# Kernel optimization log

Hardware: AMD Instinct MI355X
Metric: run time of the kernel (lower is better)

Reference implementation:

```python
import jax, jax.numpy as jnp
import numpy as np

B, S, HIST, D, NH, L = 8, 1024, 128, 1024, 16, 6
SD, TD, AD = 10, 3, 5
DH = D // NH
FF = 4 * D
EPS = 1e-5
SCALE = 1.0 / np.sqrt(DH)


def posenc(T):
    # sinusoidal PE, matches PositionalEncoding (positions start at 0)
    pos = jnp.arange(T, dtype=jnp.float32)[:, None]
    div = jnp.exp(jnp.arange(0, D, 2, dtype=jnp.float32) * (-np.log(10000.0) / D))
    pe = jnp.zeros((T, D), jnp.float32)
    pe = pe.at[:, 0::2].set(jnp.sin(pos * div))
    pe = pe.at[:, 1::2].set(jnp.cos(pos * div))
    return pe


def layernorm(x, g, b):
    m = jnp.mean(x, -1, keepdims=True)
    v = jnp.var(x, -1, keepdims=True)
    return (x - m) * jax.lax.rsqrt(v + EPS) * g + b


def mlp2(u, w1, b1, w2, b2):
    # Linear -> SiLU -> Linear (ConditionEmbedding branch)
    return jax.nn.silu(u @ w1 + b1) @ w2 + b2


def mha(q_in, kv_in, wq, bq, wk, bk, wv, bv, wo, bo, mask):
    Bq, Tq, _ = q_in.shape
    Tk = kv_in.shape[1]
    q = (q_in @ wq + bq).reshape(Bq, Tq, NH, DH)
    k = (kv_in @ wk + bk).reshape(Bq, Tk, NH, DH)
    v = (kv_in @ wv + bv).reshape(Bq, Tk, NH, DH)
    s = jnp.einsum('bthd,bshd->bhts', q, k) * SCALE + mask
    a = jax.nn.softmax(s, axis=-1)
    o = jnp.einsum('bhts,bshd->bthd', a, v).reshape(Bq, Tq, D)
    return o @ wo + bo


def setup_inputs():
    key = jax.random.key(0)
    ki = iter(jax.random.split(key, 64))
    w = lambda *sh: jax.random.normal(next(ki), sh, jnp.float32) * 0.02
    z = lambda *sh: jnp.zeros(sh, jnp.float32)
    inp = {
        'x': jax.random.normal(next(ki), (B, S, SD), jnp.float32),
        't': jax.random.randint(next(ki), (B,), 0, 30, dtype=jnp.int32),
        'target': jax.random.normal(next(ki), (B, TD), jnp.float32),
        'action': jax.random.normal(next(ki), (B, AD), jnp.float32),
        'history': jax.random.normal(next(ki), (B, HIST, SD), jnp.float32),
        'in_w': w(SD, D), 'in_b': z(D),
        't_w1': w(1, D), 't_b1': z(D), 't_w2': w(D, D), 't_b2': z(D),
        'tg_w1': w(TD, D), 'tg_b1': z(D), 'tg_w2': w(D, D), 'tg_b2': z(D),
        'ac_w1': w(AD, D), 'ac_b1': z(D), 'ac_w2': w(D, D), 'ac_b2': z(D),
        'sa_wq': w(L, D, D), 'sa_bq': z(L, D), 'sa_wk': w(L, D, D), 'sa_bk': z(L, D),
        'sa_wv': w(L, D, D), 'sa_bv': z(L, D), 'sa_wo': w(L, D, D), 'sa_bo': z(L, D),
        'ca_wq': w(L, D, D), 'ca_bq': z(L, D), 'ca_wk': w(L, D, D), 'ca_bk': z(L, D),
        'ca_wv': w(L, D, D), 'ca_bv': z(L, D), 'ca_wo': w(L, D, D), 'ca_bo': z(L, D),
        'ln1_g': jnp.ones((L, D), jnp.float32), 'ln1_b': z(L, D),
        'ln2_g': jnp.ones((L, D), jnp.float32), 'ln2_b': z(L, D),
        'ln3_g': jnp.ones((L, D), jnp.float32), 'ln3_b': z(L, D),
        'ff_w1': w(L, D, FF), 'ff_b1': z(L, FF), 'ff_w2': w(L, FF, D), 'ff_b2': z(L, D),
        'out_w': w(D, SD), 'out_b': z(SD),
    }
    return inp


def reference(x, t, target, action, history, in_w, in_b,
              t_w1, t_b1, t_w2, t_b2, tg_w1, tg_b1, tg_w2, tg_b2,
              ac_w1, ac_b1, ac_w2, ac_b2,
              sa_wq, sa_bq, sa_wk, sa_bk, sa_wv, sa_bv, sa_wo, sa_bo,
              ca_wq, ca_bq, ca_wk, ca_bk, ca_wv, ca_bv, ca_wo, ca_bo,
              ln1_g, ln1_b, ln2_g, ln2_b, ln3_g, ln3_b,
              ff_w1, ff_b1, ff_w2, ff_b2, out_w, out_b):
    # embed current traj and history (PE applied to each separately, as in torch code)
    x_emb = x @ in_w + in_b + posenc(S)[None]
    h_emb = history @ in_w + in_b + posenc(HIST)[None]
    # condition embedding: t + target + action branches
    cond = (mlp2(t[:, None].astype(jnp.float32), t_w1, t_b1, t_w2, t_b2)
            + mlp2(target, tg_w1, tg_b1, tg_w2, tg_b2)
            + mlp2(action, ac_w1, ac_b1, ac_w2, ac_b2))
    z = jnp.concatenate([h_emb, x_emb], axis=1) + cond[:, None, :]  # [B, T, D]
    T = HIST + S
    mask = jnp.where(jnp.tril(jnp.ones((T, T), bool)), 0.0, -jnp.inf)[None, None]
    mem = z  # TransformerDecoder memory is the (fixed) input sequence
    for i in range(L):
        # post-LN TransformerDecoderLayer: self-attn, cross-attn, relu FFN
        z = layernorm(z + mha(z, z, sa_wq[i], sa_bq[i], sa_wk[i], sa_bk[i],
                              sa_wv[i], sa_bv[i], sa_wo[i], sa_bo[i], mask), ln1_g[i], ln1_b[i])
        z = layernorm(z + mha(z, mem, ca_wq[i], ca_bq[i], ca_wk[i], ca_bk[i],
                              ca_wv[i], ca_bv[i], ca_wo[i], ca_bo[i], mask), ln2_g[i], ln2_b[i])
        ff = jax.nn.relu(z @ ff_w1[i] + ff_b1[i]) @ ff_w2[i] + ff_b2[i]
        z = layernorm(z + ff, ln3_g[i], ln3_b[i])
    return z[:, -S:, :] @ out_w + out_b
```

## Files before the change

### kernel.cpp

```cpp
#include <hip/hip_runtime.h>
#include <hip/hip_bf16.h>
#include <stdint.h>

#define B_    8
#define S_    1024
#define HIST_ 128
#define T_    1152
#define D_    1024
#define NH_   16
#define DH_   64
#define FF_   4096
#define L_    6
#define NROWS_ (B_*T_)

typedef __attribute__((ext_vector_type(8))) __bf16 bf16x8;
typedef __attribute__((ext_vector_type(4))) __bf16 bf16x4;
typedef __attribute__((ext_vector_type(4))) float  f32x4;

static __device__ __forceinline__ f32x4 mfma16(bf16x8 a, bf16x8 b, f32x4 c) {
  return __builtin_amdgcn_mfma_f32_16x16x32_bf16(a, b, c, 0, 0, 0);
}
static __device__ __forceinline__ void gload16(const __bf16* g, __bf16* l) {
  __builtin_amdgcn_global_load_lds((const __attribute__((address_space(1))) void*)g,
                                   (__attribute__((address_space(3))) void*)l, 16, 0, 0);
}
static __device__ __forceinline__ void gload16b(const char* g, char* l) {
  __builtin_amdgcn_global_load_lds((const __attribute__((address_space(1))) void*)g,
                                   (__attribute__((address_space(3))) void*)l, 16, 0, 0);
}
static __device__ __forceinline__ int xcd_swz(int orig, int nwg) {
  const int q = nwg >> 3, r = nwg & 7;
  const int x = orig & 7, i = orig >> 3;
  return (x < r ? x*(q+1) : r*(q+1) + (x-r)*q) + i;
}

template<int OUTMODE, int RELU>
__global__ __launch_bounds__(512, 2) void gemm256_k(const __bf16* __restrict__ A,
                                                    const __bf16* __restrict__ A2, int asplit,
                                                    const __bf16* __restrict__ Bt,
                                                    const float* __restrict__ b1,
                                                    const float* __restrict__ b2,
                                                    const float* __restrict__ b3, int s1, int s2,
                                                    void* __restrict__ CoutRM,
                                                    __bf16* __restrict__ CoutT,
                                                    int M, int N, int K, int ldc, int tsplit) {
  __shared__ __align__(16) __bf16 Lds[2][2][2][8192];
  const int tid = threadIdx.x;
  const int wid = tid >> 6, ln = tid & 63;
  const int wm = wid >> 2, wn = wid & 3;
  const int l15 = ln & 15, g = ln >> 4;
  const int nbx = N >> 8;
  const int wg = xcd_swz(blockIdx.x, gridDim.x);
  const int m0 = (wg / nbx) << 8, n0 = (wg % nbx) << 8;
  const size_t rstep = (size_t)K * 2;
  const __bf16* Aeff = (n0 < asplit) ? A : A2;

  const int srow = tid >> 2, schunk = tid & 3;
  const int sx = (schunk ^ ((srow >> 1) & 3)) << 4;
  const char* gAr = (const char*)Aeff + (size_t)(m0 + srow)*rstep + sx;
  const char* gBr = (const char*)Bt   + (size_t)(n0 + srow)*rstep + sx;
  const size_t hstep = (size_t)128 * rstep;

  const int xr = (g ^ ((l15 >> 1) & 3)) << 4;
  const int arow = l15 * 64 + xr;
  const int aoffm = (wm*128) * 64;
  const int boff  = (wn*64) * 64;

  const f32x4 zero = {0.f,0.f,0.f,0.f};
  f32x4 acc[8][4];
#pragma unroll
  for (int i=0;i<8;i++)
#pragma unroll
    for (int j=0;j<4;j++) acc[i][j] = zero;

  auto stage4 = [&](int buf, int ks, int tile) {
    const size_t off = (size_t)tile*128 + (size_t)ks*64;
    char* la = (char*)&Lds[buf][ks][0][0];
    char* lb = (char*)&Lds[buf][ks][1][0];
    gload16b(gAr + off,         la + tid*16);
    gload16b(gAr + off + hstep, la + 8192 + tid*16);
    gload16b(gBr + off,         lb + tid*16);
    gload16b(gBr + off + hstep, lb + 8192 + tid*16);
  };

  auto ktile = [&](int buf, bool st, int stile, bool gate0) {
    if (gate0) { asm volatile("s_waitcnt vmcnt(0)" ::: "memory"); }
    else       { asm volatile("s_waitcnt vmcnt(8)" ::: "memory"); }
    __builtin_amdgcn_s_barrier();
    const char* As0 = (const char*)&Lds[buf][0][0][0];
    const char* Bs0 = (const char*)&Lds[buf][0][1][0];
    const char* As1 = (const char*)&Lds[buf][1][0][0];
    const char* Bs1 = (const char*)&Lds[buf][1][1][0];
    bf16x8 a0[4], a1[4], b0[4], a2[4], b1v[4], a3[4];
#pragma unroll
    for (int mi=0;mi<4;mi++) a0[mi] = *(const bf16x8*)(As0 + aoffm + mi*1024 + arow);
#pragma unroll
    for (int ni=0;ni<4;ni++) b0[ni] = *(const bf16x8*)(Bs0 + boff + ni*1024 + arow);
#pragma unroll
    for (int mi=0;mi<4;mi++) a1[mi] = *(const bf16x8*)(As0 + aoffm + 4096 + mi*1024 + arow);
    __builtin_amdgcn_s_setprio(1);
#pragma unroll
    for (int mi=0;mi<4;mi++)
#pragma unroll
      for (int ni=0;ni<4;ni++) acc[mi][ni] = mfma16(a0[mi], b0[ni], acc[mi][ni]);
    __builtin_amdgcn_s_setprio(0);
#pragma unroll
    for (int mi=0;mi<4;mi++) a2[mi]  = *(const bf16x8*)(As1 + aoffm + mi*1024 + arow);
#pragma unroll
    for (int ni=0;ni<4;ni++) b1v[ni] = *(const bf16x8*)(Bs1 + boff + ni*1024 + arow);
    asm volatile("s_waitcnt lgkmcnt(0)" ::: "memory");
    __builtin_amdgcn_s_barrier();
    if (st) stage4(buf, 0, stile);
    __builtin_amdgcn_s_setprio(1);
#pragma unroll
    for (int mi=0;mi<4;mi++)
#pragma unroll
      for (int ni=0;ni<4;ni++) acc[4+mi][ni] = mfma16(a1[mi], b0[ni], acc[4+mi][ni]);
    __builtin_amdgcn_s_setprio(0);
#pragma unroll
    for (int mi=0;mi<4;mi++) a3[mi] = *(const bf16x8*)(As1 + aoffm + 4096 + mi*1024 + arow);
    __builtin_amdgcn_s_setprio(1);
#pragma unroll
    for (int mi=0;mi<4;mi++)
#pragma unroll
      for (int ni=0;ni<4;ni++) acc[mi][ni] = mfma16(a2[mi], b1v[ni], acc[mi][ni]);
    __builtin_amdgcn_s_setprio(0);
    asm volatile("s_waitcnt lgkmcnt(0)" ::: "memory");
    __builtin_amdgcn_s_barrier();
    if (st) stage4(buf, 1, stile);
    __builtin_amdgcn_s_setprio(1);
#pragma unroll
    for (int mi=0;mi<4;mi++)
#pragma unroll
      for (int ni=0;ni<4;ni++) acc[4+mi][ni] = mfma16(a3[mi], b1v[ni], acc[4+mi][ni]);
    __builtin_amdgcn_s_setprio(0);
  };

  stage4(0, 0, 0); stage4(0, 1, 0);
  stage4(1, 0, 1); stage4(1, 1, 1);

  const int NT = K >> 6, NI = NT >> 1;
  for (int i = 0; i < NI; ++i) {
    const bool st = (i + 1 < NI);
    ktile(0, st, 2*i + 2, false);
    ktile(1, st, 2*i + 3, i == NI - 1);
  }

  const int colb = n0 + wn*64 + l15;
#pragma unroll
  for (int mi=0;mi<8;mi++) {
    const int row = m0 + wm*128 + mi*16 + g*4;
#pragma unroll
    for (int ni=0;ni<4;ni++) {
      const int col = colb + ni*16;
      const float bv = (col < s1) ? b1[col] : ((col < s2) ? b2[col-s1] : b3[col-s2]);
      if (OUTMODE == 3 && col >= tsplit) {
        bf16x4 ct;
#pragma unroll
        for (int j=0;j<4;j++) {
          float v = acc[mi][ni][j] + bv;
          if (RELU) v = fmaxf(v, 0.f);
          ct[j] = (__bf16)v;
        }
        *(bf16x4*)(CoutT + (size_t)(col - tsplit)*M + row) = ct;
      } else {
#pragma unroll
        for (int j=0;j<4;j++) {
          float v = acc[mi][ni][j] + bv;
          if (RELU) v = fmaxf(v, 0.f);
          if (OUTMODE == 0) ((float*)CoutRM)[(size_t)(row+j)*ldc + col] = v;
          else              ((__bf16*)CoutRM)[(size_t)(row+j)*ldc + col] = (__bf16)v;
        }
      }
    }
  }
}

__global__ __launch_bounds__(256) void attn_k(const __bf16* __restrict__ QK,
                                              const __bf16* __restrict__ Vt,
                                              __bf16* __restrict__ O) {
  __shared__ __align__(16) __bf16 Ks[2][4096];
  __shared__ __align__(16) __bf16 Vs[2][4096];
  __shared__ __align__(16) __bf16 Pl[4][32*72];
  const int tid = threadIdx.x;
  const int wv = tid >> 6, ln = tid & 63;
  const int l15 = ln & 15, g = ln >> 4;
  const int wg = xcd_swz(blockIdx.x, 1152);
  const int qb = 8 - (wg % 9);
  const int hd = (wg / 9) & 15;
  const int b  = wg / 144;
  const int q0 = qb*128 + wv*32;

  bf16x8 qf[2][2];
#pragma unroll
  for (int f=0; f<2; ++f)
#pragma unroll
    for (int h=0; h<2; ++h)
      qf[f][h] = *(const bf16x8*)(QK + (size_t)(b*T_ + q0 + f*16 + l15)*2048 + hd*64 + h*32 + g*8);

  const int sr = tid >> 3;
  const int si = tid & 7;
  const int cb0 = (si*16) ^ ((sr & 7) << 4);
  const char* kg = (const char*)(QK + (size_t)b*T_*2048 + 1024 + hd*64);
  const char* vg = (const char*)(Vt + (size_t)hd*64*NROWS_ + (size_t)b*T_);

  const f32x4 zero = {0.f,0.f,0.f,0.f};
  f32x4 o[2][4];
#pragma unroll
  for (int f=0; f<2; ++f)
#pragma unroll
    for (int d=0; d<4; ++d) o[f][d] = zero;
  float mrun[2] = {-3.0e38f, -3.0e38f};
  float lrun[2] = {0.f, 0.f};
  const int nt = 2*qb + 2;

  {
    const int c = 0, kt = 0;
#pragma unroll
    for (int hr=0; hr<2; ++hr) {
      const int r = sr + hr*32;
      gload16((const __bf16*)(kg + (size_t)(kt + r)*4096 + cb0), &Ks[c][0] + hr*2048 + wv*512);
      gload16((const __bf16*)(vg + (size_t)r*(NROWS_*2) + (size_t)kt*2 + cb0), &Vs[c][0] + hr*2048 + wv*512);
    }
  }

  for (int t = 0; t < nt; ++t) {
    __syncthreads();
    if (t+1 < nt) {
      const int c = (t+1)&1, kt2 = (t+1)*64;
#pragma unroll
      for (int hr=0; hr<2; ++hr) {
        const int r = sr + hr*32;
        gload16((const __bf16*)(kg + (size_t)(kt2 + r)*4096 + cb0), &Ks[c][0] + hr*2048 + wv*512);
        gload16((const __bf16*)(vg + (size_t)r*(NROWS_*2) + (size_t)kt2*2 + cb0), &Vs[c][0] + hr*2048 + wv*512);
      }
    }
    const int kt = t*64;
    if (kt > q0 + 31) continue;
    const char* ks = (const char*)&Ks[t&1][0];
    const char* vs = (const char*)&Vs[t&1][0];

#pragma unroll
    for (int f=0; f<2; ++f) {
      const int qrow = q0 + f*16 + l15;
      f32x4 st[4];
      __builtin_amdgcn_s_setprio(1);
#pragma unroll
      for (int kf=0; kf<4; ++kf) {
        const int row = kf*16 + l15;
        const int swz = (row & 7) << 4;
        const bf16x8 k0 = *(const bf16x8*)(ks + row*128 + ((g*16) ^ swz));
        const bf16x8 k1 = *(const bf16x8*)(ks + row*128 + ((64 + g*16) ^ swz));
        st[kf] = mfma16(k1, qf[f][1], mfma16(k0, qf[f][0], zero));
      }
      __builtin_amdgcn_s_setprio(0);
      float p[16];
#pragma unroll
      for (int kf=0; kf<4; ++kf)
#pragma unroll
        for (int r=0; r<4; ++r) {
          const int kgl = kt + kf*16 + g*4 + r;
          p[kf*4+r] = (kgl <= qrow) ? st[kf][r]*0.125f : -3.0e38f;
        }
      float mloc = p[0];
#pragma unroll
      for (int i=1;i<16;i++) mloc = fmaxf(mloc, p[i]);
      mloc = fmaxf(mloc, __shfl_xor(mloc, 16));
      mloc = fmaxf(mloc, __shfl_xor(mloc, 32));
      if (__all(mloc - mrun[f] <= 8.f)) {
        float ls = 0.f;
#pragma unroll
        for (int i=0;i<16;i++) { p[i] = __expf(p[i] - mrun[f]); ls += p[i]; }
        ls += __shfl_xor(ls, 16); ls += __shfl_xor(ls, 32);
        lrun[f] += ls;
      } else {
        const float mnew = fmaxf(mrun[f], mloc);
        const float corr = __expf(mrun[f] - mnew);
        float ls = 0.f;
#pragma unroll
        for (int i=0;i<16;i++) { p[i] = __expf(p[i] - mnew); ls += p[i]; }
        ls += __shfl_xor(ls, 16); ls += __shfl_xor(ls, 32);
        lrun[f] = lrun[f]*corr + ls;
        mrun[f] = mnew;
        float cr[4];
#pragma unroll
        for (int r=0;r<4;r++) cr[r] = __shfl(corr, g*4 + r);
#pragma unroll
        for (int db=0; db<4; ++db)
#pragma unroll
          for (int r=0;r<4;r++) o[f][db][r] *= cr[r];
      }
#pragma unroll
      for (int kf=0; kf<4; ++kf) {
        bf16x4 pw;
#pragma unroll
        for (int r=0;r<4;r++) pw[r] = (__bf16)p[kf*4+r];
        *(bf16x4*)(&Pl[wv][(f*16 + l15)*72 + kf*16 + g*4]) = pw;
      }
    }
    __builtin_amdgcn_s_setprio(1);
#pragma unroll
    for (int f=0; f<2; ++f)
#pragma unroll
      for (int ks2=0; ks2<2; ++ks2) {
        const bf16x8 pa = *(const bf16x8*)(&Pl[wv][(f*16 + l15)*72 + ks2*32 + g*8]);
#pragma unroll
        for (int db=0; db<4; ++db) {
          const int d = db*16 + l15;
          const bf16x8 vf = *(const bf16x8*)(vs + d*128 + ((ks2*64 + g*16) ^ ((d & 7) << 4)));
          o[f][db] = mfma16(pa, vf, o[f][db]);
        }
      }
    __builtin_amdgcn_s_setprio(0);
  }

#pragma unroll
  for (int f=0; f<2; ++f) {
    const float inv = 1.f / lrun[f];
    float ir[4];
#pragma unroll
    for (int r=0;r<4;r++) ir[r] = __shfl(inv, g*4 + r);
#pragma unroll
    for (int db=0; db<4; ++db)
#pragma unroll
      for (int r=0;r<4;r++)
        O[(size_t)(b*T_ + q0 + f*16 + g*4 + r)*D_ + hd*64 + db*16 + l15] = (__bf16)(o[f][db][r]*ir[r]);
  }
}

__global__ __launch_bounds__(256) void wprep_k(const float* __restrict__ q, const float* __restrict__ k,
                                               const float* __restrict__ v, const float* __restrict__ o,
                                               const float* __restrict__ cq, const float* __restrict__ ck,
                                               const float* __restrict__ cv, const float* __restrict__ co,
                                               const float* __restrict__ f1, const float* __restrict__ f2,
                                               __bf16* __restrict__ wb) {
  __shared__ float tile[32][33];
  const int id = blockIdx.x;
  const float* src; __bf16* dst; int R, C, bx, by;
  if (id < 8192) {
    const int m = id >> 10, t = id & 1023; bx = t & 31; by = t >> 5;
    const float* srcs[8] = {q,k,v,o,cq,ck,cv,co};
    src = srcs[m]; dst = wb + (size_t)m*1048576; R = 1024; C = 1024;
  } else if (id < 12288) {
    const int t = id - 8192; bx = t & 127; by = t >> 7;
    src = f1; dst = wb + (size_t)8*1048576; R = 1024; C = 4096;
  } else {
    const int t = id - 12288; bx = t & 31; by = t >> 5;
    src = f2; dst = wb + (size_t)12*1048576; R = 4096; C = 1024;
  }
  const int tx = threadIdx.x & 31, ty = threadIdx.x >> 5;
  const int r0 = by*32, c0 = bx*32;
#pragma unroll
  for (int i=0;i<4;i++) tile[ty+i*8][tx] = src[(size_t)(r0+ty+i*8)*C + c0+tx];
  __syncthreads();
#pragma unroll
  for (int i=0;i<4;i++) dst[(size_t)(c0+ty+i*8)*R + r0+tx] = (__bf16)tile[tx][ty+i*8];
}

__global__ __launch_bounds__(256) void ln_k(const float* __restrict__ zin, const float* __restrict__ yin,
                                            const float* __restrict__ gam, const float* __restrict__ bet,
                                            float* __restrict__ zout, __bf16* __restrict__ zbout) {
  const int row = blockIdx.x, tid = threadIdx.x;
  const f32x4 zv = ((const f32x4*)(zin + (size_t)row*D_))[tid];
  const f32x4 yv = ((const f32x4*)(yin + (size_t)row*D_))[tid];
  f32x4 v = zv + yv;
  float s1 = v[0]+v[1]+v[2]+v[3];
  float s2 = v[0]*v[0]+v[1]*v[1]+v[2]*v[2]+v[3]*v[3];
#pragma unroll
  for (int off=32; off; off>>=1) { s1 += __shfl_xor(s1,off); s2 += __shfl_xor(s2,off); }
  __shared__ float red[8];
  const int wv = tid>>6, ln = tid&63;
  if (ln==0) { red[wv] = s1; red[4+wv] = s2; }
  __syncthreads();
  s1 = red[0]+red[1]+red[2]+red[3];
  s2 = red[4]+red[5]+red[6]+red[7];
  const float mean = s1 * (1.f/1024.f);
  const float var = s2 * (1.f/1024.f) - mean*mean;
  const float rs = rsqrtf(var + 1e-5f);
  const f32x4 gv = ((const f32x4*)gam)[tid];
  const f32x4 bv = ((const f32x4*)bet)[tid];
  f32x4 r; bf16x4 rb;
#pragma unroll
  for (int j=0;j<4;j++) { float t = (v[j]-mean)*rs*gv[j] + bv[j]; r[j] = t; rb[j] = (__bf16)t; }
  ((f32x4*)(zout + (size_t)row*D_))[tid] = r;
  ((bf16x4*)(zbout + (size_t)row*D_))[tid] = rb;
}

__global__ __launch_bounds__(256) void cond1_k(const int* __restrict__ t, const float* __restrict__ target,
                                               const float* __restrict__ action,
                                               const float* __restrict__ t_w1, const float* __restrict__ t_b1,
                                               const float* __restrict__ tg_w1, const float* __restrict__ tg_b1,
                                               const float* __restrict__ ac_w1, const float* __restrict__ ac_b1,
                                               float* __restrict__ h3) {
  const int i = blockIdx.x*256 + threadIdx.x;
  const int b = i >> 10, d = i & 1023;
  float u = (float)t[b] * t_w1[d] + t_b1[d];
  h3[i] = u / (1.f + __expf(-u));
  u = tg_b1[d];
#pragma unroll
  for (int j=0;j<3;j++) u += target[b*3+j]*tg_w1[j*1024+d];
  h3[8192 + i] = u / (1.f + __expf(-u));
  u = ac_b1[d];
#pragma unroll
  for (int j=0;j<5;j++) u += action[b*5+j]*ac_w1[j*1024+d];
  h3[16384 + i] = u / (1.f + __expf(-u));
}

__global__ __launch_bounds__(256) void cond2_k(const float* __restrict__ h3,
                                               const float* __restrict__ t_w2, const float* __restrict__ tg_w2,
                                               const float* __restrict__ ac_w2, float* __restrict__ cpart) {
  const int i = blockIdx.x*256 + threadIdx.x;
  const int ks = blockIdx.y;
  const int b = i >> 10, d = i & 1023;
  const float* ht = h3 + b*1024;
  const float* hg = h3 + 8192 + b*1024;
  const float* ha = h3 + 16384 + b*1024;
  float a = 0.f;
  for (int k = ks*128; k < ks*128+128; ++k)
    a += ht[k]*t_w2[(size_t)k*1024+d] + hg[k]*tg_w2[(size_t)k*1024+d] + ha[k]*ac_w2[(size_t)k*1024+d];
  cpart[ks*8192 + i] = a;
}

__global__ __launch_bounds__(256) void embed_k(const float* __restrict__ x, const float* __restrict__ hist,
                                               const float* __restrict__ in_w, const float* __restrict__ in_b,
                                               const float* __restrict__ cpart,
                                               const float* __restrict__ t_b2, const float* __restrict__ tg_b2,
                                               const float* __restrict__ ac_b2,
                                               float* __restrict__ z, __bf16* __restrict__ zb,
                                               __bf16* __restrict__ memb) {
  const int row = blockIdx.x, tid = threadIdx.x;
  const int b = row / T_, tt = row - b*T_;
  const float* feat = (tt < HIST_) ? (hist + ((size_t)b*HIST_ + tt)*10) : (x + ((size_t)b*S_ + (tt-HIST_))*10);
  float f[10];
#pragma unroll
  for (int s=0;s<10;s++) f[s] = feat[s];
  const float te = (float)((tt < HIST_) ? tt : tt - HIST_);
  f32x4 a = ((const f32x4*)in_b)[tid];
#pragma unroll
  for (int u=0;u<2;u++) {
    const int d = tid*4 + 2*u;
    const float freq = __expf((float)d * (-9.210340371976184f/1024.f));
    float sn, cs;
    __sincosf(te*freq, &sn, &cs);
    a[2*u] += sn; a[2*u+1] += cs;
  }
  a += ((const f32x4*)t_b2)[tid];
  a += ((const f32x4*)tg_b2)[tid];
  a += ((const f32x4*)ac_b2)[tid];
  const int cb = b*256 + tid;
#pragma unroll
  for (int ks=0;ks<8;ks++) a += ((const f32x4*)cpart)[ks*2048 + cb];
#pragma unroll
  for (int s=0;s<10;s++) {
    const f32x4 wv = ((const f32x4*)(in_w + s*1024))[tid];
    a += wv * f[s];
  }
  ((f32x4*)(z + (size_t)row*D_))[tid] = a;
  bf16x4 ab;
#pragma unroll
  for (int j=0;j<4;j++) ab[j] = (__bf16)a[j];
  ((bf16x4*)(zb + (size_t)row*D_))[tid] = ab;
  ((bf16x4*)(memb + (size_t)row*D_))[tid] = ab;
}

__global__ __launch_bounds__(256) void outp_k(const float* __restrict__ z, const float* __restrict__ w,
                                              const float* __restrict__ bo, float* __restrict__ out) {
  const int wv = threadIdx.x>>6, ln = threadIdx.x&63;
  const int row = blockIdx.x*4 + wv;
  const int b = row >> 10, s = row & 1023;
  const float* zr = z + ((size_t)b*T_ + HIST_ + s)*D_;
  float acc[10];
#pragma unroll
  for (int o=0;o<10;o++) acc[o]=0.f;
  for (int k=ln; k<1024; k+=64) {
    const float zv = zr[k];
    const float* wr = w + k*10;
#pragma unroll
    for (int o=0;o<10;o++) acc[o] += zv*wr[o];
  }
#pragma unroll
  for (int o=0;o<10;o++) {
#pragma unroll
    for (int off=32; off; off>>=1) acc[o] += __shfl_xor(acc[o], off);
  }
  if (ln==0) {
#pragma unroll
    for (int o=0;o<10;o++) out[(size_t)row*10+o] = acc[o] + bo[o];
  }
}

extern "C" void kernel_launch(void* const* d_in, const int* in_sizes, int n_in,
                              void* d_out, int out_size, void* d_ws, size_t ws_size,
                              hipStream_t stream) {
  const float* x      = (const float*)d_in[0];
  const int*   t      = (const int*)  d_in[1];
  const float* target = (const float*)d_in[2];
  const float* action = (const float*)d_in[3];
  const float* hist   = (const float*)d_in[4];
  const float* in_w   = (const float*)d_in[5];
  const float* in_b   = (const float*)d_in[6];
  const float* t_w1   = (const float*)d_in[7];
  const float* t_b1   = (const float*)d_in[8];
  const float* t_w2   = (const float*)d_in[9];
  const float* t_b2   = (const float*)d_in[10];
  const float* tg_w1  = (const float*)d_in[11];
  const float* tg_b1  = (const float*)d_in[12];
  const float* tg_w2  = (const float*)d_in[13];
  const float* tg_b2  = (const float*)d_in[14];
  const float* ac_w1  = (const float*)d_in[15];
  const float* ac_b1  = (const float*)d_in[16];
  const float* ac_w2  = (const float*)d_in[17];
  const float* ac_b2  = (const float*)d_in[18];
  const float* sa_wq  = (const float*)d_in[19];
  const float* sa_bq  = (const float*)d_in[20];
  const float* sa_wk  = (const float*)d_in[21];
  const float* sa_bk  = (const float*)d_in[22];
  const float* sa_wv  = (const float*)d_in[23];
  const float* sa_bv  = (const float*)d_in[24];
  const float* sa_wo  = (const float*)d_in[25];
  const float* sa_bo  = (const float*)d_in[26];
  const float* ca_wq  = (const float*)d_in[27];
  const float* ca_bq  = (const float*)d_in[28];
  const float* ca_wk  = (const float*)d_in[29];
  const float* ca_bk  = (const float*)d_in[30];
  const float* ca_wv  = (const float*)d_in[31];
  const float* ca_bv  = (const float*)d_in[32];
  const float* ca_wo  = (const float*)d_in[33];
  const float* ca_bo  = (const float*)d_in[34];
  const float* ln1_g  = (const float*)d_in[35];
  const float* ln1_b  = (const float*)d_in[36];
  const float* ln2_g  = (const float*)d_in[37];
  const float* ln2_b  = (const float*)d_in[38];
  const float* ln3_g  = (const float*)d_in[39];
  const float* ln3_b  = (const float*)d_in[40];
  const float* ff_w1  = (const float*)d_in[41];
  const float* ff_b1  = (const float*)d_in[42];
  const float* ff_w2  = (const float*)d_in[43];
  const float* ff_b2  = (const float*)d_in[44];
  const float* out_w  = (const float*)d_in[45];
  const float* out_b  = (const float*)d_in[46];

  if (ws_size < (size_t)224*1024*1024) return;

  char* p = (char*)d_ws;
  auto take = [&](size_t bytes) { char* r = p; p += (bytes + 255) & ~(size_t)255; return r; };
  __bf16* wbuf = (__bf16*)take((size_t)16*1024*1024*2);
  float*  z    = (float*) take((size_t)NROWS_*D_*4);
  __bf16* zb   = (__bf16*)take((size_t)NROWS_*D_*2);
  __bf16* memb = (__bf16*)take((size_t)NROWS_*D_*2);
  __bf16* qk   = (__bf16*)take((size_t)NROWS_*2048*2);
  __bf16* vt   = (__bf16*)take((size_t)1024*NROWS_*2);
  __bf16* ob   = (__bf16*)take((size_t)NROWS_*D_*2);
  float*  y    = (float*) take((size_t)NROWS_*D_*4);
  float*  h3   = (float*) take((size_t)3*8192*4);
  float*  cpart= (float*) take((size_t)8*8192*4);
  __bf16* ffh  = qk;

  const dim3 blk(256);
  const dim3 blk5(512);
  const int BIG = 1<<30;
  cond1_k<<<32, blk, 0, stream>>>(t, target, action, t_w1, t_b1, tg_w1, tg_b1, ac_w1, ac_b1, h3);
  cond2_k<<<dim3(32,8), blk, 0, stream>>>(h3, t_w2, tg_w2, ac_w2, cpart);
  embed_k<<<NROWS_, blk, 0, stream>>>(x, hist, in_w, in_b, cpart, t_b2, tg_b2, ac_b2, z, zb, memb);

  const int M = NROWS_;
  for (int li=0; li<L_; ++li) {
    const size_t w0 = (size_t)li*D_*D_, b0 = (size_t)li*D_;
    const size_t f1 = (size_t)li*D_*FF_, fb1 = (size_t)li*FF_;
    wprep_k<<<16384, blk, 0, stream>>>(sa_wq+w0, sa_wk+w0, sa_wv+w0, sa_wo+w0,
                                       ca_wq+w0, ca_wk+w0, ca_wv+w0, ca_wo+w0,
                                       ff_w1+f1, ff_w2+f1, wbuf);
    gemm256_k<3,0><<<36*12, blk5, 0, stream>>>(zb, zb, BIG, wbuf+0*1048576,
                                               sa_bq+b0, sa_bk+b0, sa_bv+b0, 1024, 2048,
                                               qk, vt, M, 3072, 1024, 2048, 2048);
    attn_k<<<1152, blk, 0, stream>>>(qk, vt, ob);
    gemm256_k<0,0><<<36*4, blk5, 0, stream>>>(ob, ob, BIG, wbuf+3*1048576,
                                              sa_bo+b0, sa_bo+b0, sa_bo+b0, BIG, BIG,
                                              y, vt, M, 1024, 1024, 1024, BIG);
    ln_k<<<NROWS_, blk, 0, stream>>>(z, y, ln1_g+b0, ln1_b+b0, z, zb);
    gemm256_k<3,0><<<36*12, blk5, 0, stream>>>(zb, memb, 1024, wbuf+4*1048576,
                                               ca_bq+b0, ca_bk+b0, ca_bv+b0, 1024, 2048,
                                               qk, vt, M, 3072, 1024, 2048, 2048);
    attn_k<<<1152, blk, 0, stream>>>(qk, vt, ob);
    gemm256_k<0,0><<<36*4, blk5, 0, stream>>>(ob, ob, BIG, wbuf+7*1048576,
                                              ca_bo+b0, ca_bo+b0, ca_bo+b0, BIG, BIG,
                                              y, vt, M, 1024, 1024, 1024, BIG);
    ln_k<<<NROWS_, blk, 0, stream>>>(z, y, ln2_g+b0, ln2_b+b0, z, zb);
    gemm256_k<1,1><<<36*16, blk5, 0, stream>>>(zb, zb, BIG, wbuf+(size_t)8*1048576,
                                               ff_b1+fb1, ff_b1+fb1, ff_b1+fb1, BIG, BIG,
                                               ffh, vt, M, 4096, 1024, 4096, BIG);
    gemm256_k<0,0><<<36*4, blk5, 0, stream>>>(ffh, ffh, BIG, wbuf+(size_t)12*1048576,
                                              ff_b2+b0, ff_b2+b0, ff_b2+b0, BIG, BIG,
                                              y, vt, M, 1024, 4096, 1024, BIG);
    ln_k<<<NROWS_, blk, 0, stream>>>(z, y, ln3_g+b0, ln3_b+b0, z, zb);
  }
  outp_k<<<2048, blk, 0, stream>>>(z, out_w, out_b, (float*)d_out);
}
```

Baseline: 4.354 ms.

## Add 192x256-tile GEMM for output/FFN projections and store residual branch in bf16

```diff
diff --git a/kernel.cpp b/kernel.cpp
--- a/kernel.cpp
+++ b/kernel.cpp
@@ -32,6 +32,112 @@
   const int q = nwg >> 3, r = nwg & 7;
   const int x = orig & 7, i = orig >> 3;
   return (x < r ? x*(q+1) : r*(q+1) + (x-r)*q) + i;
+}
+
+template<int BF16OUT, int RELU>
+__global__ __launch_bounds__(512, 2) void gemm192_k(const __bf16* __restrict__ A,
+                                                    const __bf16* __restrict__ Bt,
+                                                    const float* __restrict__ bias,
+                                                    void* __restrict__ Cout,
+                                                    int M, int N, int K, int ldc) {
+  __shared__ __align__(16) char Lds[2][57344];
+  const int tid = threadIdx.x;
+  const int wid = tid >> 6, ln = tid & 63;
+  const int wm = wid >> 2, wn = wid & 3;
+  const int l15 = ln & 15, g = ln >> 4;
+  const int nbx = N >> 8;
+  const int wg = xcd_swz(blockIdx.x, gridDim.x);
+  const int m0 = (wg / nbx) * 192, n0 = (wg % nbx) << 8;
+  const size_t rstep = (size_t)K * 2;
+
+  const char* srcp[7];
+  int dsto[7];
+#pragma unroll
+  for (int p = 0; p < 7; ++p) {
+    const int off = p*8192 + tid*16;
+    int mat, ks, row;
+    if (off < 12288)      { mat = 0; ks = 0; row = off >> 6; }
+    else if (off < 24576) { mat = 0; ks = 1; row = (off - 12288) >> 6; }
+    else if (off < 40960) { mat = 1; ks = 0; row = (off - 24576) >> 6; }
+    else                  { mat = 1; ks = 1; row = (off - 40960) >> 6; }
+    const int ch = (off >> 4) & 3;
+    const int kb = ks*64 + ((ch ^ ((row >> 1) & 3)) << 4);
+    srcp[p] = (mat ? (const char*)Bt + (size_t)(n0 + row)*rstep
+                   : (const char*)A  + (size_t)(m0 + row)*rstep) + kb;
+    dsto[p] = off;
+  }
+  auto stage = [&](int buf, int t) {
+    char* lb = &Lds[buf][0];
+    const size_t tb = (size_t)t << 7;
+#pragma unroll
+    for (int p = 0; p < 7; ++p) gload16b(srcp[p] + tb, lb + dsto[p]);
+  };
+
+  const int xr = (g ^ ((l15 >> 1) & 3)) << 4;
+  const int arow = l15*64 + xr;
+  const int aoffm = (wm*96) * 64;
+  const int boff  = 24576 + (wn*64) * 64;
+
+  const f32x4 zero = {0.f,0.f,0.f,0.f};
+  f32x4 acc[6][4];
+#pragma unroll
+  for (int i=0;i<6;i++)
+#pragma unroll
+    for (int j=0;j<4;j++) acc[i][j] = zero;
+
+  stage(0, 0); stage(1, 1);
+
+  const int NT = K >> 6;
+  for (int t = 0; t < NT; ++t) {
+    const int buf = t & 1;
+    if (t == NT-1) { asm volatile("s_waitcnt vmcnt(0)" ::: "memory"); }
+    else           { asm volatile("s_waitcnt vmcnt(7)" ::: "memory"); }
+    __builtin_amdgcn_s_barrier();
+    const char* bufp = &Lds[buf][0];
+    bf16x8 a0[6], a1[6], b0[4], b1[4];
+#pragma unroll
+    for (int mi=0;mi<6;mi++) a0[mi] = *(const bf16x8*)(bufp + aoffm + mi*1024 + arow);
+#pragma unroll
+    for (int ni=0;ni<4;ni++) b0[ni] = *(const bf16x8*)(bufp + boff + ni*1024 + arow);
+#pragma unroll
+    for (int mi=0;mi<6;mi++) a1[mi] = *(const bf16x8*)(bufp + 12288 + aoffm + mi*1024 + arow);
+    __builtin_amdgcn_s_setprio(1);
+#pragma unroll
+    for (int mi=0;mi<6;mi++)
+#pragma unroll
+      for (int ni=0;ni<4;ni++) acc[mi][ni] = mfma16(a0[mi], b0[ni], acc[mi][ni]);
+    __builtin_amdgcn_s_setprio(0);
+#pragma unroll
+    for (int ni=0;ni<4;ni++) b1[ni] = *(const bf16x8*)(bufp + boff + 16384 + ni*1024 + arow);
+    asm volatile("s_waitcnt lgkmcnt(0)" ::: "memory");
+    __builtin_amdgcn_sched_barrier(0);
+    __builtin_amdgcn_s_barrier();
+    if (t + 2 <= NT - 1) stage(buf, t + 2);
+    __builtin_amdgcn_s_setprio(1);
+#pragma unroll
+    for (int mi=0;mi<6;mi++)
+#pragma unroll
+      for (int ni=0;ni<4;ni++) acc[mi][ni] = mfma16(a1[mi], b1[ni], acc[mi][ni]);
+    __builtin_amdgcn_s_setprio(0);
+  }
+
+  const int colb = n0 + wn*64 + l15;
+#pragma unroll
+  for (int mi=0;mi<6;mi++) {
+    const int row = m0 + wm*96 + mi*16 + g*4;
+#pragma unroll
+    for (int ni=0;ni<4;ni++) {
+      const int col = colb + ni*16;
+      const float bv = bias[col];
+#pragma unroll
+      for (int j=0;j<4;j++) {
+        float v = acc[mi][ni][j] + bv;
+        if (RELU) v = fmaxf(v, 0.f);
+        if (BF16OUT) ((__bf16*)Cout)[(size_t)(row+j)*ldc + col] = (__bf16)v;
+        else         ((float*)Cout)[(size_t)(row+j)*ldc + col] = v;
+      }
+    }
+  }
 }
 
 template<int OUTMODE, int RELU>
@@ -357,13 +463,15 @@
   for (int i=0;i<4;i++) dst[(size_t)(c0+ty+i*8)*R + r0+tx] = (__bf16)tile[tx][ty+i*8];
 }
 
-__global__ __launch_bounds__(256) void ln_k(const float* __restrict__ zin, const float* __restrict__ yin,
+__global__ __launch_bounds__(256) void ln_k(const float* __restrict__ zin, const __bf16* __restrict__ yin,
                                             const float* __restrict__ gam, const float* __restrict__ bet,
                                             float* __restrict__ zout, __bf16* __restrict__ zbout) {
   const int row = blockIdx.x, tid = threadIdx.x;
   const f32x4 zv = ((const f32x4*)(zin + (size_t)row*D_))[tid];
-  const f32x4 yv = ((const f32x4*)(yin + (size_t)row*D_))[tid];
-  f32x4 v = zv + yv;
+  const bf16x4 yv4 = ((const bf16x4*)(yin + (size_t)row*D_))[tid];
+  f32x4 v;
+#pragma unroll
+  for (int j=0;j<4;j++) v[j] = zv[j] + (float)yv4[j];
   float s1 = v[0]+v[1]+v[2]+v[3];
   float s2 = v[0]*v[0]+v[1]*v[1]+v[2]*v[2]+v[3]*v[3];
 #pragma unroll
@@ -551,7 +659,7 @@
   __bf16* qk   = (__bf16*)take((size_t)NROWS_*2048*2);
   __bf16* vt   = (__bf16*)take((size_t)1024*NROWS_*2);
   __bf16* ob   = (__bf16*)take((size_t)NROWS_*D_*2);
-  float*  y    = (float*) take((size_t)NROWS_*D_*4);
+  __bf16* y    = (__bf16*)take((size_t)NROWS_*D_*2);
   float*  h3   = (float*) take((size_t)3*8192*4);
   float*  cpart= (float*) take((size_t)8*8192*4);
   __bf16* ffh  = qk;
@@ -574,24 +682,16 @@
                                                sa_bq+b0, sa_bk+b0, sa_bv+b0, 1024, 2048,
                                                qk, vt, M, 3072, 1024, 2048, 2048);
     attn_k<<<1152, blk, 0, stream>>>(qk, vt, ob);
-    gemm256_k<0,0><<<36*4, blk5, 0, stream>>>(ob, ob, BIG, wbuf+3*1048576,
-                                              sa_bo+b0, sa_bo+b0, sa_bo+b0, BIG, BIG,
-                                              y, vt, M, 1024, 1024, 1024, BIG);
+    gemm192_k<1,0><<<48*4, blk5, 0, stream>>>(ob, wbuf+3*1048576, sa_bo+b0, y, M, 1024, 1024, 1024);
     ln_k<<<NROWS_, blk, 0, stream>>>(z, y, ln1_g+b0, ln1_b+b0, z, zb);
     gemm256_k<3,0><<<36*12, blk5, 0, stream>>>(zb, memb, 1024, wbuf+4*1048576,
                                                ca_bq+b0, ca_bk+b0, ca_bv+b0, 1024, 2048,
                                                qk, vt, M, 3072, 1024, 2048, 2048);
     attn_k<<<1152, blk, 0, stream>>>(qk, vt, ob);
-    gemm256_k<0,0><<<36*4, blk5, 0, stream>>>(ob, ob, BIG, wbuf+7*1048576,
-                                              ca_bo+b0, ca_bo+b0, ca_bo+b0, BIG, BIG,
-                                              y, vt, M, 1024, 1024, 1024, BIG);
+    gemm192_k<1,0><<<48*4, blk5, 0, stream>>>(ob, wbuf+7*1048576, ca_bo+b0, y, M, 1024, 1024, 1024);
     ln_k<<<NROWS_, blk, 0, stream>>>(z, y, ln2_g+b0, ln2_b+b0, z, zb);
-    gemm256_k<1,1><<<36*16, blk5, 0, stream>>>(zb, zb, BIG, wbuf+(size_t)8*1048576,
-                                               ff_b1+fb1, ff_b1+fb1, ff_b1+fb1, BIG, BIG,
-                                               ffh, vt, M, 4096, 1024, 4096, BIG);
-    gemm256_k<0,0><<<36*4, blk5, 0, stream>>>(ffh, ffh, BIG, wbuf+(size_t)12*1048576,
-                                              ff_b2+b0, ff_b2+b0, ff_b2+b0, BIG, BIG,
-                                              y, vt, M, 1024, 4096, 1024, BIG);
+    gemm192_k<1,1><<<48*16, blk5, 0, stream>>>(zb, wbuf+(size_t)8*1048576, ff_b1+fb1, ffh, M, 4096, 1024, 4096);
+    gemm192_k<1,0><<<48*4, blk5, 0, stream>>>(ffh, wbuf+(size_t)12*1048576, ff_b2+b0, y, M, 1024, 4096, 1024);
     ln_k<<<NROWS_, blk, 0, stream>>>(z, y, ln3_g+b0, ln3_b+b0, z, zb);
   }
   outp_k<<<2048, blk, 0, stream>>>(z, out_w, out_b, (float*)d_out);
```

Result: faster. 3.947 ms (-9.4%).

## Switch GEMM to 192x256 tiles and store residual GEMM output in bf16

Applied to the files above, without the earlier changes.

```diff
diff --git a/kernel.cpp b/kernel.cpp
--- a/kernel.cpp
+++ b/kernel.cpp
@@ -35,7 +35,7 @@
 }
 
 template<int OUTMODE, int RELU>
-__global__ __launch_bounds__(512, 2) void gemm256_k(const __bf16* __restrict__ A,
+__global__ __launch_bounds__(512, 2) void gemm192_k(const __bf16* __restrict__ A,
                                                     const __bf16* __restrict__ A2, int asplit,
                                                     const __bf16* __restrict__ Bt,
                                                     const float* __restrict__ b1,
@@ -44,112 +44,92 @@
                                                     void* __restrict__ CoutRM,
                                                     __bf16* __restrict__ CoutT,
                                                     int M, int N, int K, int ldc, int tsplit) {
-  __shared__ __align__(16) __bf16 Lds[2][2][2][8192];
+  __shared__ __align__(16) char Lds[2][57344];
   const int tid = threadIdx.x;
   const int wid = tid >> 6, ln = tid & 63;
   const int wm = wid >> 2, wn = wid & 3;
   const int l15 = ln & 15, g = ln >> 4;
   const int nbx = N >> 8;
   const int wg = xcd_swz(blockIdx.x, gridDim.x);
-  const int m0 = (wg / nbx) << 8, n0 = (wg % nbx) << 8;
+  const int m0 = (wg / nbx) * 192, n0 = (wg % nbx) << 8;
   const size_t rstep = (size_t)K * 2;
   const __bf16* Aeff = (n0 < asplit) ? A : A2;
 
-  const int srow = tid >> 2, schunk = tid & 3;
-  const int sx = (schunk ^ ((srow >> 1) & 3)) << 4;
-  const char* gAr = (const char*)Aeff + (size_t)(m0 + srow)*rstep + sx;
-  const char* gBr = (const char*)Bt   + (size_t)(n0 + srow)*rstep + sx;
-  const size_t hstep = (size_t)128 * rstep;
+  const char* srcp[7];
+  int dsto[7];
+#pragma unroll
+  for (int p = 0; p < 7; ++p) {
+    const int off = p*8192 + tid*16;
+    int mat, ks, row;
+    if (off < 12288)      { mat = 0; ks = 0; row = off >> 6; }
+    else if (off < 24576) { mat = 0; ks = 1; row = (off - 12288) >> 6; }
+    else if (off < 40960) { mat = 1; ks = 0; row = (off - 24576) >> 6; }
+    else                  { mat = 1; ks = 1; row = (off - 40960) >> 6; }
+    const int ch = (off >> 4) & 3;
+    const int kb = ks*64 + ((ch ^ ((row >> 1) & 3)) << 4);
+    srcp[p] = (mat ? (const char*)Bt   + (size_t)(n0 + row)*rstep
+                   : (const char*)Aeff + (size_t)(m0 + row)*rstep) + kb;
+    dsto[p] = off;
+  }
+  auto stage = [&](int buf, int t) {
+    char* lb = &Lds[buf][0];
+    const size_t tb = (size_t)t << 7;
+#pragma unroll
+    for (int p = 0; p < 7; ++p) gload16b(srcp[p] + tb, lb + dsto[p]);
+  };
 
   const int xr = (g ^ ((l15 >> 1) & 3)) << 4;
-  const int arow = l15 * 64 + xr;
-  const int aoffm = (wm*128) * 64;
-  const int boff  = (wn*64) * 64;
+  const int arow = l15*64 + xr;
+  const int aoffm = (wm*96) * 64;
+  const int boff  = 24576 + (wn*64) * 64;
 
   const f32x4 zero = {0.f,0.f,0.f,0.f};
-  f32x4 acc[8][4];
-#pragma unroll
-  for (int i=0;i<8;i++)
+  f32x4 acc[6][4];
+#pragma unroll
+  for (int i=0;i<6;i++)
 #pragma unroll
     for (int j=0;j<4;j++) acc[i][j] = zero;
 
-  auto stage4 = [&](int buf, int ks, int tile) {
-    const size_t off = (size_t)tile*128 + (size_t)ks*64;
-    char* la = (char*)&Lds[buf][ks][0][0];
-    char* lb = (char*)&Lds[buf][ks][1][0];
-    gload16b(gAr + off,         la + tid*16);
-    gload16b(gAr + off + hstep, la + 8192 + tid*16);
-    gload16b(gBr + off,         lb + tid*16);
-    gload16b(gBr + off + hstep, lb + 8192 + tid*16);
-  };
-
-  auto ktile = [&](int buf, bool st, int stile, bool gate0) {
-    if (gate0) { asm volatile("s_waitcnt vmcnt(0)" ::: "memory"); }
-    else       { asm volatile("s_waitcnt vmcnt(8)" ::: "memory"); }
+  stage(0, 0); stage(1, 1);
+
+  const int NT = K >> 6;
+  for (int t = 0; t < NT; ++t) {
+    const int buf = t & 1;
+    if (t == NT-1) { asm volatile("s_waitcnt vmcnt(0)" ::: "memory"); }
+    else           { asm volatile("s_waitcnt vmcnt(7)" ::: "memory"); }
     __builtin_amdgcn_s_barrier();
-    const char* As0 = (const char*)&Lds[buf][0][0][0];
-    const char* Bs0 = (const char*)&Lds[buf][0][1][0];
-    const char* As1 = (const char*)&Lds[buf][1][0][0];
-    const char* Bs1 = (const char*)&Lds[buf][1][1][0];
-    bf16x8 a0[4], a1[4], b0[4], a2[4], b1v[4], a3[4];
-#pragma unroll
-    for (int mi=0;mi<4;mi++) a0[mi] = *(const bf16x8*)(As0 + aoffm + mi*1024 + arow);
-#pragma unroll
-    for (int ni=0;ni<4;ni++) b0[ni] = *(const bf16x8*)(Bs0 + boff + ni*1024 + arow);
-#pragma unroll
-    for (int mi=0;mi<4;mi++) a1[mi] = *(const bf16x8*)(As0 + aoffm + 4096 + mi*1024 + arow);
+    const char* bufp = &Lds[buf][0];
+    bf16x8 a0[6], a1[6], b0[4], b1[4];
+#pragma unroll
+    for (int mi=0;mi<6;mi++) a0[mi] = *(const bf16x8*)(bufp + aoffm + mi*1024 + arow);
+#pragma unroll
+    for (int ni=0;ni<4;ni++) b0[ni] = *(const bf16x8*)(bufp + boff + ni*1024 + arow);
+#pragma unroll
+    for (int mi=0;mi<6;mi++) a1[mi] = *(const bf16x8*)(bufp + 12288 + aoffm + mi*1024 + arow);
     __builtin_amdgcn_s_setprio(1);
 #pragma unroll
-    for (int mi=0;mi<4;mi++)
+    for (int mi=0;mi<6;mi++)
 #pragma unroll
       for (int ni=0;ni<4;ni++) acc[mi][ni] = mfma16(a0[mi], b0[ni], acc[mi][ni]);
     __builtin_amdgcn_s_setprio(0);
 #pragma unroll
-    for (int mi=0;mi<4;mi++) a2[mi]  = *(const bf16x8*)(As1 + aoffm + mi*1024 + arow);
-#pragma unroll
-    for (int ni=0;ni<4;ni++) b1v[ni] = *(const bf16x8*)(Bs1 + boff + ni*1024 + arow);
+    for (int ni=0;ni<4;ni++) b1[ni] = *(const bf16x8*)(bufp + boff + 16384 + ni*1024 + arow);
     asm volatile("s_waitcnt lgkmcnt(0)" ::: "memory");
+    __builtin_amdgcn_sched_barrier(0);
     __builtin_amdgcn_s_barrier();
-    if (st) stage4(buf, 0, stile);
+    if (t + 2 <= NT - 1) stage(buf, t + 2);
     __builtin_amdgcn_s_setprio(1);
 #pragma unroll
-    for (int mi=0;mi<4;mi++)
-#pragma unroll
-      for (int ni=0;ni<4;ni++) acc[4+mi][ni] = mfma16(a1[mi], b0[ni], acc[4+mi][ni]);
+    for (int mi=0;mi<6;mi++)
+#pragma unroll
+      for (int ni=0;ni<4;ni++) acc[mi][ni] = mfma16(a1[mi], b1[ni], acc[mi][ni]);
     __builtin_amdgcn_s_setprio(0);
-#pragma unroll
-    for (int mi=0;mi<4;mi++) a3[mi] = *(const bf16x8*)(As1 + aoffm + 4096 + mi*1024 + arow);
-    __builtin_amdgcn_s_setprio(1);
-#pragma unroll
-    for (int mi=0;mi<4;mi++)
-#pragma unroll
-      for (int ni=0;ni<4;ni++) acc[mi][ni] = mfma16(a2[mi], b1v[ni], acc[mi][ni]);
-    __builtin_amdgcn_s_setprio(0);
-    asm volatile("s_waitcnt lgkmcnt(0)" ::: "memory");
-    __builtin_amdgcn_s_barrier();
-    if (st) stage4(buf, 1, stile);
-    __builtin_amdgcn_s_setprio(1);
-#pragma unroll
-    for (int mi=0;mi<4;mi++)
-#pragma unroll
-      for (int ni=0;ni<4;ni++) acc[4+mi][ni] = mfma16(a3[mi], b1v[ni], acc[4+mi][ni]);
-    __builtin_amdgcn_s_setprio(0);
-  };
-
-  stage4(0, 0, 0); stage4(0, 1, 0);
-  stage4(1, 0, 1); stage4(1, 1, 1);
-
-  const int NT = K >> 6, NI = NT >> 1;
-  for (int i = 0; i < NI; ++i) {
-    const bool st = (i + 1 < NI);
-    ktile(0, st, 2*i + 2, false);
-    ktile(1, st, 2*i + 3, i == NI - 1);
   }
 
   const int colb = n0 + wn*64 + l15;
 #pragma unroll
-  for (int mi=0;mi<8;mi++) {
-    const int row = m0 + wm*128 + mi*16 + g*4;
+  for (int mi=0;mi<6;mi++) {
+    const int row = m0 + wm*96 + mi*16 + g*4;
 #pragma unroll
     for (int ni=0;ni<4;ni++) {
       const int col = colb + ni*16;
@@ -357,13 +337,15 @@
   for (int i=0;i<4;i++) dst[(size_t)(c0+ty+i*8)*R + r0+tx] = (__bf16)tile[tx][ty+i*8];
 }
 
-__global__ __launch_bounds__(256) void ln_k(const float* __restrict__ zin, const float* __restrict__ yin,
+__global__ __launch_bounds__(256) void ln_k(const float* __restrict__ zin, const __bf16* __restrict__ yin,
                                             const float* __restrict__ gam, const float* __restrict__ bet,
                                             float* __restrict__ zout, __bf16* __restrict__ zbout) {
   const int row = blockIdx.x, tid = threadIdx.x;
   const f32x4 zv = ((const f32x4*)(zin + (size_t)row*D_))[tid];
-  const f32x4 yv = ((const f32x4*)(yin + (size_t)row*D_))[tid];
-  f32x4 v = zv + yv;
+  const bf16x4 yv4 = ((const bf16x4*)(yin + (size_t)row*D_))[tid];
+  f32x4 v;
+#pragma unroll
+  for (int j=0;j<4;j++) v[j] = zv[j] + (float)yv4[j];
   float s1 = v[0]+v[1]+v[2]+v[3];
   float s2 = v[0]*v[0]+v[1]*v[1]+v[2]*v[2]+v[3]*v[3];
 #pragma unroll
@@ -551,7 +533,7 @@
   __bf16* qk   = (__bf16*)take((size_t)NROWS_*2048*2);
   __bf16* vt   = (__bf16*)take((size_t)1024*NROWS_*2);
   __bf16* ob   = (__bf16*)take((size_t)NROWS_*D_*2);
-  float*  y    = (float*) take((size_t)NROWS_*D_*4);
+  __bf16* y    = (__bf16*)take((size_t)NROWS_*D_*2);
   float*  h3   = (float*) take((size_t)3*8192*4);
   float*  cpart= (float*) take((size_t)8*8192*4);
   __bf16* ffh  = qk;
@@ -570,26 +552,26 @@
     wprep_k<<<16384, blk, 0, stream>>>(sa_wq+w0, sa_wk+w0, sa_wv+w0, sa_wo+w0,
                                        ca_wq+w0, ca_wk+w0, ca_wv+w0, ca_wo+w0,
                                        ff_w1+f1, ff_w2+f1, wbuf);
-    gemm256_k<3,0><<<36*12, blk5, 0, stream>>>(zb, zb, BIG, wbuf+0*1048576,
+    gemm192_k<3,0><<<48*12, blk5, 0, stream>>>(zb, zb, BIG, wbuf+0*1048576,
                                                sa_bq+b0, sa_bk+b0, sa_bv+b0, 1024, 2048,
                                                qk, vt, M, 3072, 1024, 2048, 2048);
     attn_k<<<1152, blk, 0, stream>>>(qk, vt, ob);
-    gemm256_k<0,0><<<36*4, blk5, 0, stream>>>(ob, ob, BIG, wbuf+3*1048576,
+    gemm192_k<1,0><<<48*4, blk5, 0, stream>>>(ob, ob, BIG, wbuf+3*1048576,
                                               sa_bo+b0, sa_bo+b0, sa_bo+b0, BIG, BIG,
                                               y, vt, M, 1024, 1024, 1024, BIG);
     ln_k<<<NROWS_, blk, 0, stream>>>(z, y, ln1_g+b0, ln1_b+b0, z, zb);
-    gemm256_k<3,0><<<36*12, blk5, 0, stream>>>(zb, memb, 1024, wbuf+4*1048576,
+    gemm192_k<3,0><<<48*12, blk5, 0, stream>>>(zb, memb, 1024, wbuf+4*1048576,
                                                ca_bq+b0, ca_bk+b0, ca_bv+b0, 1024, 2048,
                                                qk, vt, M, 3072, 1024, 2048, 2048);
     attn_k<<<1152, blk, 0, stream>>>(qk, vt, ob);
-    gemm256_k<0,0><<<36*4, blk5, 0, stream>>>(ob, ob, BIG, wbuf+7*1048576,
+    gemm192_k<1,0><<<48*4, blk5, 0, stream>>>(ob, ob, BIG, wbuf+7*1048576,
                                               ca_bo+b0, ca_bo+b0, ca_bo+b0, BIG, BIG,
                                               y, vt, M, 1024, 1024, 1024, BIG);
     ln_k<<<NROWS_, blk, 0, stream>>>(z, y, ln2_g+b0, ln2_b+b0, z, zb);
-    gemm256_k<1,1><<<36*16, blk5, 0, stream>>>(zb, zb, BIG, wbuf+(size_t)8*1048576,
+    gemm192_k<1,1><<<48*16, blk5, 0, stream>>>(zb, zb, BIG, wbuf+(size_t)8*1048576,
                                                ff_b1+fb1, ff_b1+fb1, ff_b1+fb1, BIG, BIG,
                                                ffh, vt, M, 4096, 1024, 4096, BIG);
-    gemm256_k<0,0><<<36*4, blk5, 0, stream>>>(ffh, ffh, BIG, wbuf+(size_t)12*1048576,
+    gemm192_k<1,0><<<48*4, blk5, 0, stream>>>(ffh, ffh, BIG, wbuf+(size_t)12*1048576,
                                               ff_b2+b0, ff_b2+b0, ff_b2+b0, BIG, BIG,
                                               y, vt, M, 1024, 4096, 1024, BIG);
     ln_k<<<NROWS_, blk, 0, stream>>>(z, y, ln3_g+b0, ln3_b+b0, z, zb);
```

New measurement: 4.162 ms. 4.4% less time.
